# Kernel optimization log

Measured on AMD Instinct MI355X. Metric: run time of the kernel, lower is better.

## Reference

```python
import jax, jax.numpy as jnp
import numpy as np

B, L, E, H = 8, 2048, 768, 512

def setup_inputs() -> dict:
    key = jax.random.key(0)
    ks = jax.random.split(key, 12)
    s = 0.05
    rn = lambda k, shp: jax.random.normal(k, shp, dtype=jnp.float32) * s
    return {
        "embedded_inputs": jax.random.normal(ks[0], (B, L, E), dtype=jnp.float32),
        "decoder_input_init": jax.random.normal(ks[1], (B, H), dtype=jnp.float32),
        "W_ih": rn(ks[2], (4 * H, E)), "W_hh": rn(ks[3], (4 * H, H)),
        "b_ih": jnp.zeros((4 * H,), jnp.float32), "b_hh": jnp.zeros((4 * H,), jnp.float32),
        "Wd_in": rn(ks[4], (4 * H, H)), "bd_in": jnp.zeros((4 * H,), jnp.float32),
        "Wd_hh": rn(ks[5], (4 * H, H)), "bd_hh": jnp.zeros((4 * H,), jnp.float32),
        "W_inp": rn(ks[6], (H, H)), "b_inp": jnp.zeros((H,), jnp.float32),
        "Wc": rn(ks[7], (H, H)), "bc": jnp.zeros((H,), jnp.float32),
        "V": jax.random.uniform(ks[8], (H,), minval=-1.0, maxval=1.0, dtype=jnp.float32),
        "W_out": rn(ks[9], (H, 2 * H)), "b_out": jnp.zeros((H,), jnp.float32),
    }


def _lstm_cell(x, h, c, W_in, b_in, W_hid, b_hid):
    # gates chunked in (input, forget, cell, out) order, matching torch .chunk(4,1)
    g = x @ W_in.T + b_in + h @ W_hid.T + b_hid
    i, f, gc, o = jnp.split(g, 4, axis=-1)
    c_t = jax.nn.sigmoid(f) * c + jax.nn.sigmoid(i) * jnp.tanh(gc)
    h_t = jax.nn.sigmoid(o) * jnp.tanh(c_t)
    return h_t, c_t


def _encode(x, W_ih, W_hh, b_ih, b_hh):
    # x: [B, L, E] -> outputs [B, L, H], last (h, c)
    Hh = W_hh.shape[1]
    h0 = jnp.zeros((x.shape[0], Hh), x.dtype)
    def step(carry, xt):
        h, c = carry
        h, c = _lstm_cell(xt, h, c, W_ih, b_ih, W_hh, b_hh)
        return (h, c), h
    (hT, cT), outs = jax.lax.scan(step, (h0, h0), x.transpose(1, 0, 2))
    return outs.transpose(1, 0, 2), hT, cT


def reference(embedded_inputs, decoder_input_init, W_ih, W_hh, b_ih, b_hh,
              Wd_in, bd_in, Wd_hh, bd_hh, W_inp, b_inp, Wc, bc, V, W_out, b_out):
    enc_out, h, c = _encode(embedded_inputs, W_ih, W_hh, b_ih, b_hh)  # [B,L,H]
    context = enc_out
    Bc, Lc = context.shape[0], context.shape[1]
    # Conv1d(k=1) over permuted context == per-position linear -> ctx [B,H,L]
    ctx = jnp.einsum('blh,oh->bol', context, Wc) + bc[None, :, None]
    mask = jnp.ones((Bc, Lc), context.dtype)
    x = decoder_input_init
    outputs, pointers = [], []
    for _ in range(2):  # source decodes exactly 2 pointers (start/end)
        h_t, c = _lstm_cell(x, h, c, Wd_in, bd_in, Wd_hh, bd_hh)
        inp = (h_t @ W_inp.T + b_inp)[:, :, None]                 # [B,H,1]
        att = jnp.einsum('h,bhl->bl', V, jnp.tanh(inp + ctx))     # [B,L]
        att = jnp.where(mask == 0, -jnp.inf, att)
        alpha = jax.nn.softmax(att, axis=1)
        hidden_state = jnp.einsum('bhl,bl->bh', ctx, alpha)
        h = jnp.tanh(jnp.concatenate([hidden_state, h_t], axis=-1) @ W_out.T + b_out)
        idx = jnp.argmax(alpha * mask, axis=1)
        onehot = jax.nn.one_hot(idx, Lc, dtype=mask.dtype)
        mask = mask * (1.0 - onehot)
        x = jnp.take_along_axis(enc_out, idx[:, None, None], axis=1)[:, 0, :]
        outputs.append(alpha)
        pointers.append(idx)
    return jnp.stack(outputs, axis=1), jnp.stack(pointers, axis=1)
```

## Files before the change

### kernel.cpp

```cpp
#include <hip/hip_runtime.h>
#include <math.h>

#define B_   8
#define L_   2048
#define E_   768
#define H_   512
#define G4_  2048
#define CL_  512

static __device__ __forceinline__ float sigm(float x){ return 1.0f/(1.0f+expf(-x)); }

__global__ __launch_bounds__(256) void gemm128(
    const float* __restrict__ A, const float* __restrict__ W,
    const float* __restrict__ bias1, const float* __restrict__ bias2,
    float* __restrict__ C, int M, int N, int K, int CL, int Ltot, int c0)
{
  __shared__ float As[16][132];
  __shared__ float Bs[16][132];
  const int tid = threadIdx.x;
  const int bm = blockIdx.y * 128, bn = blockIdx.x * 128;

  const int r  = tid >> 1;
  const int kq = (tid & 1) * 8;
  const int am = bm + r;
  const int ab = am / CL, al = am % CL;
  const float* Arow = A + ((size_t)ab * Ltot + c0 + al) * K;
  const float* Wrow = W + (size_t)(bn + r) * K;

  const int tx = tid & 15, ty = tid >> 4;
  float acc[8][8] = {};

  for (int k0 = 0; k0 < K; k0 += 16) {
    float4 a0 = *(const float4*)(Arow + k0 + kq);
    float4 a1 = *(const float4*)(Arow + k0 + kq + 4);
    float4 w0 = *(const float4*)(Wrow + k0 + kq);
    float4 w1 = *(const float4*)(Wrow + k0 + kq + 4);
    __syncthreads();
    As[kq+0][r]=a0.x; As[kq+1][r]=a0.y; As[kq+2][r]=a0.z; As[kq+3][r]=a0.w;
    As[kq+4][r]=a1.x; As[kq+5][r]=a1.y; As[kq+6][r]=a1.z; As[kq+7][r]=a1.w;
    Bs[kq+0][r]=w0.x; Bs[kq+1][r]=w0.y; Bs[kq+2][r]=w0.z; Bs[kq+3][r]=w0.w;
    Bs[kq+4][r]=w1.x; Bs[kq+5][r]=w1.y; Bs[kq+6][r]=w1.z; Bs[kq+7][r]=w1.w;
    __syncthreads();
    #pragma unroll
    for (int k = 0; k < 16; ++k) {
      float4 x0 = *(const float4*)&As[k][ty*4];
      float4 x1 = *(const float4*)&As[k][64 + ty*4];
      float4 y0 = *(const float4*)&Bs[k][tx*4];
      float4 y1 = *(const float4*)&Bs[k][64 + tx*4];
      float av[8] = {x0.x,x0.y,x0.z,x0.w, x1.x,x1.y,x1.z,x1.w};
      float bv[8] = {y0.x,y0.y,y0.z,y0.w, y1.x,y1.y,y1.z,y1.w};
      #pragma unroll
      for (int i=0;i<8;++i)
        #pragma unroll
        for (int j=0;j<8;++j)
          acc[i][j] += av[i]*bv[j];
    }
  }

  float bs[8];
  #pragma unroll
  for (int j=0;j<4;++j) {
    int c0n = bn + tx*4 + j, c1n = bn + 64 + tx*4 + j;
    bs[j]   = bias1[c0n] + (bias2 ? bias2[c0n] : 0.0f);
    bs[4+j] = bias1[c1n] + (bias2 ? bias2[c1n] : 0.0f);
  }
  #pragma unroll
  for (int i=0;i<8;++i) {
    int row = bm + ((i<4) ? (ty*4+i) : (64 + ty*4 + (i-4)));
    float4 o0 = { acc[i][0]+bs[0], acc[i][1]+bs[1], acc[i][2]+bs[2], acc[i][3]+bs[3] };
    float4 o1 = { acc[i][4]+bs[4], acc[i][5]+bs[5], acc[i][6]+bs[6], acc[i][7]+bs[7] };
    *(float4*)&C[(size_t)row*N + bn + tx*4]      = o0;
    *(float4*)&C[(size_t)row*N + bn + 64 + tx*4] = o1;
  }
}

__global__ __launch_bounds__(256, 1) void recur2(
    const float* __restrict__ Xp,
    const float* __restrict__ Whh,
    float* __restrict__ enc_out,
    unsigned long long* __restrict__ hb2,
    float* __restrict__ cbuf,
    float* __restrict__ hT,
    int t0, int nsteps)
{
  const int tid = threadIdx.x;
  const int b   = blockIdx.x & 7;
  const int m   = blockIdx.x >> 3;
  const int c   = tid >> 4, q = tid & 15;
  const int gi_c = c >> 2;
  const int jb   = (c & 3) * 8;

  __shared__ float hsh[512];
  __shared__ float gsum[128];
  __shared__ float xpsh[128];

  float4 w4[8][8];
  #pragma unroll
  for (int r = 0; r < 8; ++r) {
    const float* wr = Whh + ((size_t)(gi_c*H_ + m*32 + jb + r))*H_ + q*4;
    #pragma unroll
    for (int k = 0; k < 8; ++k) w4[r][k] = *(const float4*)(wr + k*64);
  }
  float cc = 0.0f;
  if (tid < 32) cc = cbuf[b*H_ + m*32 + tid];

  for (int s = 0; s < nsteps; ++s) {
    const int t = t0 + s;
    float xv = 0.0f;
    if (tid < 128)
      xv = Xp[((size_t)(b*CL_ + s))*G4_ + (size_t)(tid>>5)*H_ + m*32 + (tid&31)];

    {
      const unsigned long long* src =
          hb2 + ((size_t)(t & 1))*(B_*H_) + (size_t)b*H_ + tid*2;
      unsigned long long v0 = 0, v1 = 0;
      bool d0 = false, d1 = false;
      do {
        if (!d0) v0 = __hip_atomic_load(src,   __ATOMIC_RELAXED, __HIP_MEMORY_SCOPE_AGENT);
        if (!d1) v1 = __hip_atomic_load(src+1, __ATOMIC_RELAXED, __HIP_MEMORY_SCOPE_AGENT);
        d0 = d0 || ((unsigned)(v0 >> 32) == (unsigned)t);
        d1 = d1 || ((unsigned)(v1 >> 32) == (unsigned)t);
      } while (!(d0 && d1));
      union { unsigned u; float f; } a0, a1;
      a0.u = (unsigned)v0; a1.u = (unsigned)v1;
      hsh[2*tid]   = a0.f;
      hsh[2*tid+1] = a1.f;
      if (tid < 128) xpsh[tid] = xv;
    }
    __syncthreads();

    float acc[8] = {0,0,0,0,0,0,0,0};
    #pragma unroll
    for (int k = 0; k < 8; ++k) {
      float4 h4 = *(const float4*)&hsh[q*4 + k*64];
      #pragma unroll
      for (int r = 0; r < 8; ++r) {
        acc[r] = fmaf(w4[r][k].x, h4.x, acc[r]);
        acc[r] = fmaf(w4[r][k].y, h4.y, acc[r]);
        acc[r] = fmaf(w4[r][k].z, h4.z, acc[r]);
        acc[r] = fmaf(w4[r][k].w, h4.w, acc[r]);
      }
    }
    #pragma unroll
    for (int msk = 1; msk < 16; msk <<= 1)
      #pragma unroll
      for (int r = 0; r < 8; ++r) acc[r] += __shfl_xor(acc[r], msk, 64);
    if (q < 8) gsum[c*8 + q] = acc[q];
    __syncthreads();

    if (tid < 32) {
      float g0 = gsum[tid]      + xpsh[tid];
      float g1 = gsum[32 + tid] + xpsh[32 + tid];
      float g2 = gsum[64 + tid] + xpsh[64 + tid];
      float g3 = gsum[96 + tid] + xpsh[96 + tid];
      cc = sigm(g1)*cc + sigm(g0)*tanhf(g2);
      float hn = sigm(g3)*tanhf(cc);
      const int j = m*32 + tid;
      union { float f; unsigned u; } hu; hu.f = hn;
      unsigned long long wv =
          (((unsigned long long)(unsigned)(t + 1)) << 32) | (unsigned long long)hu.u;
      __hip_atomic_store(hb2 + ((size_t)((t+1) & 1))*(B_*H_) + (size_t)b*H_ + j, wv,
                         __ATOMIC_RELAXED, __HIP_MEMORY_SCOPE_AGENT);
      enc_out[((size_t)b*L_ + t)*H_ + j] = hn;
      if (t == L_ - 1) hT[b*H_ + j] = hn;
    }
    __syncthreads();
  }
  if (tid < 32) cbuf[b*H_ + m*32 + tid] = cc;
}

__global__ __launch_bounds__(256) void dual_mv(
    const float* __restrict__ x1, const float* __restrict__ W1, int ld1, int K1,
    const float* __restrict__ x2, const float* __restrict__ W2, int ld2, int K2,
    const float* __restrict__ bias1, const float* __restrict__ bias2,
    float* __restrict__ out, int N, int act)
{
  const int w = blockIdx.x*4 + (threadIdx.x>>6);
  const int lane = threadIdx.x & 63;
  const int b = w / N, n = w % N;
  float s = 0.0f;
  for (int k = lane*4; k < K1; k += 256) {
    float4 xv = *(const float4*)(x1 + (size_t)b*K1 + k);
    float4 wv = *(const float4*)(W1 + (size_t)n*ld1 + k);
    s += xv.x*wv.x + xv.y*wv.y + xv.z*wv.z + xv.w*wv.w;
  }
  if (x2) {
    for (int k = lane*4; k < K2; k += 256) {
      float4 xv = *(const float4*)(x2 + (size_t)b*K2 + k);
      float4 wv = *(const float4*)(W2 + (size_t)n*ld2 + k);
      s += xv.x*wv.x + xv.y*wv.y + xv.z*wv.z + xv.w*wv.w;
    }
  }
  #pragma unroll
  for (int m=32; m>0; m>>=1) s += __shfl_xor(s, m, 64);
  if (lane == 0) {
    float r = s + bias1[n] + (bias2 ? bias2[n] : 0.0f);
    if (act) r = tanhf(r);
    out[(size_t)b*N + n] = r;
  }
}

__global__ void dec_cell(const float* __restrict__ g, float* __restrict__ c,
                         float* __restrict__ ht)
{
  int i = blockIdx.x*256 + threadIdx.x;
  int b = i >> 9, j = i & 511;
  const float* gb = g + (size_t)b*G4_;
  float gi_ = gb[j], gf = gb[H_+j], gg = gb[2*H_+j], go = gb[3*H_+j];
  float cc = c[i];
  cc = sigm(gf)*cc + sigm(gi_)*tanhf(gg);
  ht[i] = sigm(go)*tanhf(cc);
  c[i]  = cc;
}

__global__ __launch_bounds__(256) void dec_att(
    const float* __restrict__ inp, const float* __restrict__ ctx,
    const float* __restrict__ V, float* __restrict__ att)
{
  const int w = blockIdx.x*4 + (threadIdx.x>>6);
  const int lane = threadIdx.x & 63;
  const int b = w >> 11;
  const float* cr = ctx + (size_t)w*H_;
  const float* ip = inp + (size_t)b*H_;
  float s = 0.0f;
  #pragma unroll
  for (int i=0;i<2;++i) {
    int k = lane*4 + i*256;
    float4 c4 = *(const float4*)(cr+k);
    float4 i4 = *(const float4*)(ip+k);
    float4 v4 = *(const float4*)(V+k);
    s += v4.x*tanhf(i4.x+c4.x) + v4.y*tanhf(i4.y+c4.y)
       + v4.z*tanhf(i4.z+c4.z) + v4.w*tanhf(i4.w+c4.w);
  }
  #pragma unroll
  for (int m=32; m>0; m>>=1) s += __shfl_xor(s, m, 64);
  if (lane == 0) att[w] = s;
}

__global__ __launch_bounds__(256) void dec_softmax(
    const float* __restrict__ att, const float* __restrict__ enc,
    int iter, int* __restrict__ chosen,
    float* __restrict__ out_alpha, float* __restrict__ out_ptr,
    float* __restrict__ x_next)
{
  const int b = blockIdx.x, tid = threadIdx.x;
  __shared__ float rv[256]; __shared__ int ri[256];
  __shared__ float s_mx, s_sum; __shared__ int s_idx;
  const int banned = iter ? chosen[b] : -1;
  float a[8]; float mx = -INFINITY;
  #pragma unroll
  for (int i=0;i<8;++i) {
    int l = (i<<8)+tid;
    float v = att[(size_t)b*L_ + l];
    if (l == banned) v = -INFINITY;
    a[i] = v; mx = fmaxf(mx, v);
  }
  rv[tid]=mx; __syncthreads();
  for (int s=128;s>0;s>>=1){ if (tid<s) rv[tid]=fmaxf(rv[tid],rv[tid+s]); __syncthreads(); }
  if (tid==0) s_mx = rv[0];
  __syncthreads();
  const float MX = s_mx;
  __syncthreads();
  float sum = 0.0f;
  #pragma unroll
  for (int i=0;i<8;++i) {
    int l = (i<<8)+tid;
    float pexp = (l == banned) ? 0.0f : expf(a[i]-MX);
    sum += pexp; a[i] = pexp;
  }
  rv[tid]=sum; __syncthreads();
  for (int s=128;s>0;s>>=1){ if (tid<s) rv[tid]+=rv[tid+s]; __syncthreads(); }
  if (tid==0) s_sum = rv[0];
  __syncthreads();
  const float inv = 1.0f/s_sum;
  __syncthreads();
  float vb = -1.0f; int ib = 1<<30;
  #pragma unroll
  for (int i=0;i<8;++i) {
    int l = (i<<8)+tid;
    if (l != banned) { float v = a[i]; if (v > vb || (v == vb && l < ib)) { vb=v; ib=l; } }
  }
  rv[tid]=vb; ri[tid]=ib; __syncthreads();
  for (int s=128;s>0;s>>=1) {
    if (tid<s) {
      float v2=rv[tid+s]; int i2=ri[tid+s];
      if (v2 > rv[tid] || (v2 == rv[tid] && i2 < ri[tid])) { rv[tid]=v2; ri[tid]=i2; }
    }
    __syncthreads();
  }
  if (tid==0) {
    s_idx = ri[0];
    out_ptr[b*2+iter] = (float)ri[0];
    if (iter==0) chosen[b] = ri[0];
  }
  __syncthreads();
  #pragma unroll
  for (int i=0;i<8;++i) {
    int l = (i<<8)+tid;
    out_alpha[((size_t)b*2+iter)*L_ + l] = a[i]*inv;
  }
  const int idx = s_idx;
  for (int j=tid; j<H_; j+=256)
    x_next[(size_t)b*H_ + j] = enc[((size_t)b*L_ + idx)*H_ + j];
}

__global__ void dec_hidden1(const float* __restrict__ ctx, const float* __restrict__ alpha_all,
                            int iter, float* __restrict__ part)
{
  const int b = blockIdx.x >> 4, ch = blockIdx.x & 15;
  const int j = threadIdx.x;
  const float* al = alpha_all + ((size_t)b*2+iter)*L_ + ch*128;
  const float* cp = ctx + ((size_t)b*L_ + ch*128)*H_ + j;
  float s = 0.0f;
  for (int l=0; l<128; ++l) s += cp[(size_t)l*H_] * al[l];
  part[((size_t)b*16+ch)*H_ + j] = s;
}

__global__ void dec_hidden2(const float* __restrict__ part, float* __restrict__ hid)
{
  int i = blockIdx.x*256 + threadIdx.x;
  int b = i >> 9, j = i & 511;
  float s = 0.0f;
  #pragma unroll
  for (int ch=0; ch<16; ++ch) s += part[((size_t)b*16+ch)*H_ + j];
  hid[i] = s;
}

extern "C" void kernel_launch(void* const* d_in, const int* in_sizes, int n_in,
                              void* d_out, int out_size, void* d_ws, size_t ws_size,
                              hipStream_t stream)
{
  const float* emb   = (const float*)d_in[0];
  const float* x0    = (const float*)d_in[1];
  const float* W_ih  = (const float*)d_in[2];
  const float* W_hh  = (const float*)d_in[3];
  const float* b_ih  = (const float*)d_in[4];
  const float* b_hh  = (const float*)d_in[5];
  const float* Wd_in = (const float*)d_in[6];
  const float* bd_in = (const float*)d_in[7];
  const float* Wd_hh = (const float*)d_in[8];
  const float* bd_hh = (const float*)d_in[9];
  const float* W_inp = (const float*)d_in[10];
  const float* b_inp = (const float*)d_in[11];
  const float* Wc    = (const float*)d_in[12];
  const float* bc    = (const float*)d_in[13];
  const float* V     = (const float*)d_in[14];
  const float* W_out = (const float*)d_in[15];
  const float* b_out = (const float*)d_in[16];

  float* ws  = (float*)d_ws;
  float* XP  = ws;
  float* CTX = ws;
  float* ENC = XP + (size_t)8388608;
  unsigned long long* HB2 = (unsigned long long*)(ENC + (size_t)8388608);
  float* HB  = (float*)(HB2 + 8192);
  float* CB  = HB + 4096;
  float* DG  = CB + 4096;
  float* HT  = DG + 16384;
  float* INP = HT + 4096;
  float* ATT = INP + 4096;
  float* HID = ATT + 16384;
  float* XN  = HID + 4096;
  float* HD  = XN + 4096;
  float* PART = HD + 4096;
  int* CHOSEN = (int*)(PART + 65536);

  hipMemsetAsync(HB2, 0, 8192*sizeof(unsigned long long) + (4096+4096)*sizeof(float), stream);

  for (int c=0; c<4; ++c) {
    gemm128<<<dim3(G4_/128, (B_*CL_)/128), 256, 0, stream>>>(
        emb, W_ih, b_ih, b_hh, XP, B_*CL_, G4_, E_, CL_, L_, c*CL_);
    recur2<<<128, 256, 0, stream>>>(XP, W_hh, ENC, HB2, CB, HB, c*CL_, CL_);
  }
  gemm128<<<dim3(H_/128, (B_*L_)/128), 256, 0, stream>>>(
      ENC, Wc, bc, nullptr, CTX, B_*L_, H_, H_, L_, L_, 0);

  float* out = (float*)d_out;
  const float* x_cur = x0;
  const float* h_cur = HB;
  for (int iter=0; iter<2; ++iter) {
    dual_mv<<<(B_*G4_)/4, 256, 0, stream>>>(x_cur, Wd_in, H_, H_,
                                            h_cur, Wd_hh, H_, H_,
                                            bd_in, bd_hh, DG, G4_, 0);
    dec_cell<<<16, 256, 0, stream>>>(DG, CB, HT);
    dual_mv<<<(B_*H_)/4, 256, 0, stream>>>(HT, W_inp, H_, H_,
                                           nullptr, nullptr, 0, 0,
                                           b_inp, nullptr, INP, H_, 0);
    dec_att<<<(B_*L_)/4, 256, 0, stream>>>(INP, CTX, V, ATT);
    dec_softmax<<<B_, 256, 0, stream>>>(ATT, ENC, iter, CHOSEN, out, out + 32768, XN);
    dec_hidden1<<<B_*16, 512, 0, stream>>>(CTX, out, iter, PART);
    dec_hidden2<<<16, 256, 0, stream>>>(PART, HID);
    dual_mv<<<(B_*H_)/4, 256, 0, stream>>>(HID, W_out, 2*H_, H_,
                                           HT, W_out + H_, 2*H_, H_,
                                           b_out, nullptr, HD, H_, 1);
    x_cur = XN; h_cur = HD;
  }
}
```

Measured before the change: 5.999 ms.

## Double-buffer LSTM recurrence shared state and drop trailing barrier

The recurrent kernel now double-buffers its shared h, gate-sum and input-projection arrays by step parity, which lets it remove the third __syncthreads per timestep. The threads whose h slice is produced by their own block skip polling global memory after the first step and read the value written directly into shared memory. This shortens the serial per-step critical path of the 2048-step recurrence. It relies on the parity buffering to keep correctness with one fewer barrier.

```diff
diff --git a/kernel.cpp b/kernel.cpp
--- a/kernel.cpp
+++ b/kernel.cpp
@@ -74,7 +74,7 @@
   }
 }
 
-__global__ __launch_bounds__(256, 1) void recur2(
+__global__ __launch_bounds__(256, 1) void recur3(
     const float* __restrict__ Xp,
     const float* __restrict__ Whh,
     float* __restrict__ enc_out,
@@ -86,13 +86,13 @@
   const int tid = threadIdx.x;
   const int b   = blockIdx.x & 7;
   const int m   = blockIdx.x >> 3;
-  const int c   = tid >> 4, q = tid & 15;
-  const int gi_c = c >> 2;
-  const int jb   = (c & 3) * 8;
-
-  __shared__ float hsh[512];
-  __shared__ float gsum[128];
-  __shared__ float xpsh[128];
+  const int cq  = tid >> 4, q = tid & 15;
+  const int gi_c = cq >> 2;
+  const int jb   = (cq & 3) * 8;
+
+  __shared__ float hsh[2][512];
+  __shared__ float gsum[2][128];
+  __shared__ float xpsh[2][128];
 
   float4 w4[8][8];
   #pragma unroll
@@ -104,13 +104,17 @@
   float cc = 0.0f;
   if (tid < 32) cc = cbuf[b*H_ + m*32 + tid];
 
+  const bool ownPoll = ((tid >> 4) == m);
+
   for (int s = 0; s < nsteps; ++s) {
     const int t = t0 + s;
+    const int p = s & 1;
+
     float xv = 0.0f;
     if (tid < 128)
       xv = Xp[((size_t)(b*CL_ + s))*G4_ + (size_t)(tid>>5)*H_ + m*32 + (tid&31)];
 
-    {
+    if (!(ownPoll && s > 0)) {
       const unsigned long long* src =
           hb2 + ((size_t)(t & 1))*(B_*H_) + (size_t)b*H_ + tid*2;
       unsigned long long v0 = 0, v1 = 0;
@@ -123,16 +127,16 @@
       } while (!(d0 && d1));
       union { unsigned u; float f; } a0, a1;
       a0.u = (unsigned)v0; a1.u = (unsigned)v1;
-      hsh[2*tid]   = a0.f;
-      hsh[2*tid+1] = a1.f;
-      if (tid < 128) xpsh[tid] = xv;
-    }
+      hsh[p][2*tid]   = a0.f;
+      hsh[p][2*tid+1] = a1.f;
+    }
+    if (tid < 128) xpsh[p][tid] = xv;
     __syncthreads();
 
     float acc[8] = {0,0,0,0,0,0,0,0};
     #pragma unroll
     for (int k = 0; k < 8; ++k) {
-      float4 h4 = *(const float4*)&hsh[q*4 + k*64];
+      float4 h4 = *(const float4*)&hsh[p][q*4 + k*64];
       #pragma unroll
       for (int r = 0; r < 8; ++r) {
         acc[r] = fmaf(w4[r][k].x, h4.x, acc[r]);
@@ -145,14 +149,14 @@
     for (int msk = 1; msk < 16; msk <<= 1)
       #pragma unroll
       for (int r = 0; r < 8; ++r) acc[r] += __shfl_xor(acc[r], msk, 64);
-    if (q < 8) gsum[c*8 + q] = acc[q];
+    if (q < 8) gsum[p][cq*8 + q] = acc[q];
     __syncthreads();
 
     if (tid < 32) {
-      float g0 = gsum[tid]      + xpsh[tid];
-      float g1 = gsum[32 + tid] + xpsh[32 + tid];
-      float g2 = gsum[64 + tid] + xpsh[64 + tid];
-      float g3 = gsum[96 + tid] + xpsh[96 + tid];
+      float g0 = gsum[p][tid]      + xpsh[p][tid];
+      float g1 = gsum[p][32 + tid] + xpsh[p][32 + tid];
+      float g2 = gsum[p][64 + tid] + xpsh[p][64 + tid];
+      float g3 = gsum[p][96 + tid] + xpsh[p][96 + tid];
       cc = sigm(g1)*cc + sigm(g0)*tanhf(g2);
       float hn = sigm(g3)*tanhf(cc);
       const int j = m*32 + tid;
@@ -161,10 +165,10 @@
           (((unsigned long long)(unsigned)(t + 1)) << 32) | (unsigned long long)hu.u;
       __hip_atomic_store(hb2 + ((size_t)((t+1) & 1))*(B_*H_) + (size_t)b*H_ + j, wv,
                          __ATOMIC_RELAXED, __HIP_MEMORY_SCOPE_AGENT);
+      hsh[p^1][j] = hn;
       enc_out[((size_t)b*L_ + t)*H_ + j] = hn;
       if (t == L_ - 1) hT[b*H_ + j] = hn;
     }
-    __syncthreads();
   }
   if (tid < 32) cbuf[b*H_ + m*32 + tid] = cc;
 }
@@ -370,7 +374,7 @@
   for (int c=0; c<4; ++c) {
     gemm128<<<dim3(G4_/128, (B_*CL_)/128), 256, 0, stream>>>(
         emb, W_ih, b_ih, b_hh, XP, B_*CL_, G4_, E_, CL_, L_, c*CL_);
-    recur2<<<128, 256, 0, stream>>>(XP, W_hh, ENC, HB2, CB, HB, c*CL_, CL_);
+    recur3<<<128, 256, 0, stream>>>(XP, W_hh, ENC, HB2, CB, HB, c*CL_, CL_);
   }
   gemm128<<<dim3(H_/128, (B_*L_)/128), 256, 0, stream>>>(
       ENC, Wc, bc, nullptr, CTX, B_*L_, H_, H_, L_, L_, 0);
```

Result: faster. 5.740 ms (-4.3%).
